# Kernel tuning notes

Measured on AMD Instinct MI355X. Metric: run time of the kernel, lower is better.

Reference implementation:

```python
import jax, jax.numpy as jnp
import numpy as np

H = 4  # pairwise_num_attention_heads

def _layer_norm(x, gamma, beta, eps=1e-5):
    mu = jnp.mean(x, axis=-1, keepdims=True)
    var = jnp.var(x, axis=-1, keepdims=True)
    return (x - mu) * jax.lax.rsqrt(var + eps) * gamma + beta

def setup_inputs() -> dict:
    key = jax.random.key(0)
    ks = jax.random.split(key, 8)
    B, L, P = 1, 256, 128
    s = 0.02
    return {
        "pairwise_states": jax.random.normal(ks[0], (B, L, L, P), jnp.float32),
        "ln_gamma": jnp.ones((P,), jnp.float32),
        "ln_beta": jnp.zeros((P,), jnp.float32),
        "Wq": jax.random.normal(ks[1], (P, P), jnp.float32) * s,
        "Wk": jax.random.normal(ks[2], (P, P), jnp.float32) * s,
        "Wv": jax.random.normal(ks[3], (P, P), jnp.float32) * s,
        "Wb": jax.random.normal(ks[4], (P, H), jnp.float32) * s,
        "Wg": jax.random.normal(ks[5], (P, P), jnp.float32) * s,
        "bg": jnp.zeros((P,), jnp.float32),
        "Wo": jax.random.normal(ks[6], (P, P), jnp.float32) * s,
        "bo": jnp.zeros((P,), jnp.float32),
    }

def reference(pairwise_states, ln_gamma, ln_beta, Wq, Wk, Wv, Wb, Wg, bg, Wo, bo):
    # Row-axis triangle attention (RibonanzaNetPairwiseAttention, axis='row', eval mode).
    B, L, _, P = pairwise_states.shape
    D = P // H  # attention_head_size
    x = _layer_norm(pairwise_states, ln_gamma, ln_beta)  # [b,i,j,p]
    q = (x @ Wq).reshape(B, L, L, H, D)
    k = (x @ Wk).reshape(B, L, L, H, D)
    v = (x @ Wv).reshape(B, L, L, H, D)
    scale = jnp.asarray(D, x.dtype) ** 0.5
    # pairwise bias: [b,i,j,h] -> broadcast over the row axis of the scores
    bias = jnp.einsum('bijp,ph->bhij', x, Wb)  # [b,h,L,L]
    # scores[b,h,i,j,k]: within row i, query position j attends to key position k
    scores = jnp.einsum('bijhd,bikhd->bhijk', q, k) / scale + bias[:, :, None]
    probs = jax.nn.softmax(scores, axis=-1)
    ctx = jnp.einsum('bhijk,bikhd->bijhd', probs, v).reshape(B, L, L, P)
    gate = jax.nn.sigmoid(x @ Wg + bg)
    ctx = gate * ctx
    # output dense + residual (AxisDropout is identity in eval mode)
    return ctx @ Wo + bo + pairwise_states
```

## Files before the change

kernel.cpp:

```cpp
#include <hip/hip_runtime.h>

#define NPOS 65536

typedef __attribute__((ext_vector_type(8))) short bf16x8;
typedef __attribute__((ext_vector_type(4))) float f32x4;

#if __has_builtin(__builtin_amdgcn_exp2f)
#define EXP2F(x) __builtin_amdgcn_exp2f(x)
#else
#define EXP2F(x) __expf((x) * 0.6931471805599453f)
#endif
#if __has_builtin(__builtin_amdgcn_rcpf)
#define RCPF(x) __builtin_amdgcn_rcpf(x)
#else
#define RCPF(x) (1.0f / (x))
#endif

static __device__ __forceinline__ unsigned short f2bf(float f) {
  union { float f; unsigned int u; } v; v.f = f;
  unsigned int r = v.u + 0x7fffu + ((v.u >> 16) & 1u);
  return (unsigned short)(r >> 16);
}
static __device__ __forceinline__ float lo_bf(unsigned int u) {
  union { unsigned int u; float f; } v; v.u = u << 16; return v.f;
}
static __device__ __forceinline__ float hi_bf(unsigned int u) {
  union { unsigned int u; float f; } v; v.u = u & 0xffff0000u; return v.f;
}
static __device__ __forceinline__ unsigned int permpack(float hi, float lo) {
  union { float f; unsigned int u; } a, b;
  a.f = hi; b.f = lo;
#if __has_builtin(__builtin_amdgcn_perm)
  return __builtin_amdgcn_perm(a.u, b.u, 0x07060302u);
#else
  return (a.u & 0xffff0000u) | (b.u >> 16);
#endif
}

__global__ void k_pack(const float* __restrict__ Wq, const float* __restrict__ Wk,
                       const float* __restrict__ Wv, const float* __restrict__ Wg,
                       const float* __restrict__ Wo,
                       ushort* __restrict__ WT, ushort* __restrict__ WoT) {
  int idx = blockIdx.x * blockDim.x + threadIdx.x;
  if (idx < 512 * 128) {
    int n = idx >> 7, k = idx & 127;
    int nn = n & 127;
    float val;
    if (n < 128)      val = Wq[k * 128 + nn] * (0.17677669529663687f * 1.4426950408889634f);
    else if (n < 256) val = Wk[k * 128 + nn];
    else if (n < 384) val = Wv[k * 128 + nn];
    else              val = Wg[k * 128 + nn];
    WT[idx] = f2bf(val);
  } else if (idx < 512 * 128 + 128 * 128) {
    int j = idx - 512 * 128;
    int n = j >> 7, k = j & 127;
    WoT[j] = f2bf(Wo[k * 128 + n]);
  }
}

__global__ __launch_bounds__(128, 4) void k_ln(
    const float* __restrict__ in, const float* __restrict__ gamma,
    const float* __restrict__ beta, const float* __restrict__ Wb,
    ushort* __restrict__ xln, ushort* __restrict__ biasB) {
  int t = threadIdx.x, wv = t >> 6, lane = t & 63;
  int n = lane & 15, g = lane >> 4;
  int myrow = blockIdx.x * 32 + wv * 16 + n;
  const float* rp = in + (size_t)myrow * 128;

  float xv[32];
  float sm = 0.f, ssm = 0.f;
  #pragma unroll
  for (int kc = 0; kc < 4; kc++)
    #pragma unroll
    for (int pr = 0; pr < 2; pr++) {
      float4 v = *(const float4*)(rp + kc * 32 + g * 8 + pr * 4);
      int o = kc * 8 + pr * 4;
      xv[o] = v.x; xv[o+1] = v.y; xv[o+2] = v.z; xv[o+3] = v.w;
      sm  += v.x + v.y + v.z + v.w;
      ssm += v.x*v.x + v.y*v.y + v.z*v.z + v.w*v.w;
    }
  sm  += __shfl_xor(sm, 16, 64);  sm  += __shfl_xor(sm, 32, 64);
  ssm += __shfl_xor(ssm, 16, 64); ssm += __shfl_xor(ssm, 32, 64);
  float mu  = sm * (1.0f / 128.0f);
  float var = ssm * (1.0f / 128.0f) - mu * mu;
  float rs  = rsqrtf(var + 1e-5f);
  float p0 = 0.f, p1 = 0.f, p2 = 0.f, p3 = 0.f;
  #pragma unroll
  for (int kc = 0; kc < 4; kc++)
    #pragma unroll
    for (int pr = 0; pr < 2; pr++) {
      int c0 = kc * 32 + g * 8 + pr * 4;
      float4 g4 = *(const float4*)(gamma + c0);
      float4 b4 = *(const float4*)(beta + c0);
      int o = kc * 8 + pr * 4;
      #pragma unroll
      for (int r = 0; r < 4; r++) {
        float xn = (xv[o + r] - mu) * rs * (&g4.x)[r] + (&b4.x)[r];
        xv[o + r] = xn;
        float4 w = ((const float4*)Wb)[c0 + r];
        p0 += xn * w.x; p1 += xn * w.y; p2 += xn * w.z; p3 += xn * w.w;
      }
    }
  #pragma unroll
  for (int kc = 0; kc < 4; kc++)
    #pragma unroll
    for (int pr = 0; pr < 2; pr++) {
      int o = kc * 8 + pr * 4;
      uint2 px;
      px.x = (unsigned int)f2bf(xv[o]) | ((unsigned int)f2bf(xv[o + 1]) << 16);
      px.y = (unsigned int)f2bf(xv[o + 2]) | ((unsigned int)f2bf(xv[o + 3]) << 16);
      *(uint2*)(xln + (size_t)myrow * 128 + kc * 32 + g * 8 + pr * 4) = px;
    }
  p0 += __shfl_xor(p0, 16, 64); p0 += __shfl_xor(p0, 32, 64);
  p1 += __shfl_xor(p1, 16, 64); p1 += __shfl_xor(p1, 32, 64);
  p2 += __shfl_xor(p2, 16, 64); p2 += __shfl_xor(p2, 32, 64);
  p3 += __shfl_xor(p3, 16, 64); p3 += __shfl_xor(p3, 32, 64);
  if (g == 0) {
    const float l2e = 1.4426950408889634f;
    biasB[0 * NPOS + myrow] = f2bf(p0 * l2e);
    biasB[1 * NPOS + myrow] = f2bf(p1 * l2e);
    biasB[2 * NPOS + myrow] = f2bf(p2 * l2e);
    biasB[3 * NPOS + myrow] = f2bf(p3 * l2e);
  }
}

#define KS 40
#define VS 264
#define PST 40
__global__ __launch_bounds__(512, 2) void k_attn2(
    const ushort* __restrict__ xln, const ushort* __restrict__ WT,
    const float* __restrict__ bg, const ushort* __restrict__ biasB,
    ushort* __restrict__ gctx) {
  __shared__ __align__(16) ushort Klds[256 * KS];
  __shared__ __align__(16) ushort VTlds[32 * VS];
  __shared__ __align__(16) ushort pstg[8][16 * PST];
  int i = blockIdx.x & 255, h = blockIdx.x >> 8;
  int t = threadIdx.x, wv = t >> 6, lane = t & 63;
  int n = lane & 15, g = lane >> 4;
  int r0 = wv * 32;

  bf16x8 a[2][4];
  const ushort* xb = xln + ((size_t)i * 256 + r0) * 128;
  #pragma unroll
  for (int c = 0; c < 2; c++)
    #pragma unroll
    for (int kc = 0; kc < 4; kc++)
      a[c][kc] = *(const bf16x8*)(xb + (size_t)(c * 16 + n) * 128 + kc * 32 + g * 8);

  bf16x8 qreg[2];
  f32x4 gs[2][2];
  #pragma unroll
  for (int sect = 0; sect < 4; sect++) {
    bf16x8 b[2][4];
    #pragma unroll
    for (int ntl = 0; ntl < 2; ntl++)
      #pragma unroll
      for (int kc = 0; kc < 4; kc++)
        b[ntl][kc] = *(const bf16x8*)(WT + (size_t)(sect * 128 + h * 32 + ntl * 16 + n) * 128 + kc * 32 + g * 8);
    #pragma unroll
    for (int c = 0; c < 2; c++) {
      f32x4 acc[2];
      #pragma unroll
      for (int ntl = 0; ntl < 2; ntl++) {
        f32x4 cc = {0.f, 0.f, 0.f, 0.f};
        #pragma unroll
        for (int kc = 0; kc < 4; kc++) {
          if (sect == 0)
            cc = __builtin_amdgcn_mfma_f32_16x16x32_bf16(b[ntl][kc], a[c][kc], cc, 0, 0, 0);
          else
            cc = __builtin_amdgcn_mfma_f32_16x16x32_bf16(a[c][kc], b[ntl][kc], cc, 0, 0, 0);
        }
        acc[ntl] = cc;
      }
      if (sect == 0) {
        union { bf16x8 v; uint2 u[2]; } q;
        q.u[0].x = permpack(acc[0][1], acc[0][0]);
        q.u[0].y = permpack(acc[0][3], acc[0][2]);
        q.u[1].x = permpack(acc[1][1], acc[1][0]);
        q.u[1].y = permpack(acc[1][3], acc[1][2]);
        qreg[c] = q.v;
      } else if (sect == 1) {
        #pragma unroll
        for (int ntl = 0; ntl < 2; ntl++)
          #pragma unroll
          for (int r = 0; r < 4; r++)
            Klds[(r0 + c * 16 + g * 4 + r) * KS + ntl * 16 + n] = f2bf(acc[ntl][r]);
      } else if (sect == 2) {
        #pragma unroll
        for (int ntl = 0; ntl < 2; ntl++) {
          uint2 vp;
          vp.x = (unsigned int)f2bf(acc[ntl][0]) | ((unsigned int)f2bf(acc[ntl][1]) << 16);
          vp.y = (unsigned int)f2bf(acc[ntl][2]) | ((unsigned int)f2bf(acc[ntl][3]) << 16);
          *(uint2*)(&VTlds[(ntl * 16 + n) * VS + r0 + c * 16 + g * 4]) = vp;
        }
      } else {
        #pragma unroll
        for (int ntl = 0; ntl < 2; ntl++)
          #pragma unroll
          for (int r = 0; r < 4; r++)
            gs[c][ntl][r] = 1.0f / (1.0f + __expf(-(acc[ntl][r] + bg[h * 32 + ntl * 16 + n])));
      }
    }
  }
  __syncthreads();

  const ushort* bb = biasB + (size_t)h * NPOS;
  ushort* Pw = pstg[wv];
  #pragma unroll
  for (int tt = 0; tt < 2; tt++) {
    int j0 = r0 + tt * 16;
    uint2 bv[16];
    #pragma unroll
    for (int kt = 0; kt < 16; kt++)
      bv[kt] = *(const uint2*)(bb + (size_t)(j0 + n) * 256 + kt * 16 + g * 4);
    f32x4 s[16];
    #pragma unroll
    for (int kt = 0; kt < 16; kt++) {
      union { bf16x8 v; uint2 u[2]; } ak;
      ak.u[0] = *(const uint2*)(&Klds[(kt * 16 + n) * KS + g * 4]);
      ak.u[1] = *(const uint2*)(&Klds[(kt * 16 + n) * KS + 16 + g * 4]);
      f32x4 cc;
      cc[0] = lo_bf(bv[kt].x); cc[1] = hi_bf(bv[kt].x);
      cc[2] = lo_bf(bv[kt].y); cc[3] = hi_bf(bv[kt].y);
      s[kt] = __builtin_amdgcn_mfma_f32_16x16x32_bf16(ak.v, qreg[tt], cc, 0, 0, 0);
    }
    f32x4 a4 = {0.f, 0.f, 0.f, 0.f};
    #pragma unroll
    for (int kt = 0; kt < 16; kt++) {
      #pragma unroll
      for (int r = 0; r < 4; r++) s[kt][r] = EXP2F(s[kt][r]);
      a4 += s[kt];
    }
    float smm = (a4[0] + a4[1]) + (a4[2] + a4[3]);
    smm += __shfl_xor(smm, 16, 64);
    smm += __shfl_xor(smm, 32, 64);
    float inv = RCPF(smm);
    f32x4 ctx0 = {0.f, 0.f, 0.f, 0.f}, ctx1 = {0.f, 0.f, 0.f, 0.f};
    #pragma unroll
    for (int c8 = 0; c8 < 8; c8++) {
      #pragma unroll
      for (int t2 = 0; t2 < 2; t2++) {
        int kt = c8 * 2 + t2;
        uint2 pp;
        pp.x = permpack(s[kt][1] * inv, s[kt][0] * inv);
        pp.y = permpack(s[kt][3] * inv, s[kt][2] * inv);
        *(uint2*)(&Pw[n * PST + t2 * 16 + g * 4]) = pp;
      }
      bf16x8 ap = *(const bf16x8*)(&Pw[n * PST + g * 8]);
      bf16x8 v0 = *(const bf16x8*)(&VTlds[(size_t)n * VS + c8 * 32 + g * 8]);
      bf16x8 v1 = *(const bf16x8*)(&VTlds[(size_t)(16 + n) * VS + c8 * 32 + g * 8]);
      ctx0 = __builtin_amdgcn_mfma_f32_16x16x32_bf16(ap, v0, ctx0, 0, 0, 0);
      ctx1 = __builtin_amdgcn_mfma_f32_16x16x32_bf16(ap, v1, ctx1, 0, 0, 0);
    }
    #pragma unroll
    for (int r = 0; r < 4; r++) {
      size_t pos = (size_t)i * 256 + j0 + g * 4 + r;
      gctx[pos * 128 + h * 32 + n]      = f2bf(ctx0[r] * gs[tt][0][r]);
      gctx[pos * 128 + h * 32 + 16 + n] = f2bf(ctx1[r] * gs[tt][1][r]);
    }
  }
}

__global__ __launch_bounds__(256, 4) void k_out(
    const ushort* __restrict__ gctx, const ushort* __restrict__ WoT,
    const float* __restrict__ bo, const float* __restrict__ in0,
    float* __restrict__ out) {
  int t = threadIdx.x, wv = t >> 6, lane = t & 63;
  int n = lane & 15, g = lane >> 4;
  int row0 = blockIdx.x * 64 + wv * 16;
  bf16x8 cfr[4];
  #pragma unroll
  for (int kc = 0; kc < 4; kc++)
    cfr[kc] = *(const bf16x8*)(gctx + (size_t)(row0 + n) * 128 + kc * 32 + g * 8);
  size_t rowg = (size_t)row0 + n;
  #pragma unroll
  for (int ntl = 0; ntl < 8; ntl++) {
    f32x4 acc = {0.f, 0.f, 0.f, 0.f};
    #pragma unroll
    for (int kc = 0; kc < 4; kc++) {
      bf16x8 wo = *(const bf16x8*)(WoT + (size_t)(ntl * 16 + n) * 128 + kc * 32 + g * 8);
      acc = __builtin_amdgcn_mfma_f32_16x16x32_bf16(wo, cfr[kc], acc, 0, 0, 0);
    }
    f32x4 b4 = *(const f32x4*)(bo + ntl * 16 + g * 4);
    size_t o = rowg * 128 + ntl * 16 + g * 4;
    f32x4 r4 = *(const f32x4*)(in0 + o);
    acc[0] += b4[0] + r4[0]; acc[1] += b4[1] + r4[1];
    acc[2] += b4[2] + r4[2]; acc[3] += b4[3] + r4[3];
    *(f32x4*)(out + o) = acc;
  }
}

extern "C" void kernel_launch(void* const* d_in, const int* in_sizes, int n_in,
                              void* d_out, int out_size, void* d_ws, size_t ws_size,
                              hipStream_t stream) {
  const float* in0   = (const float*)d_in[0];
  const float* gamma = (const float*)d_in[1];
  const float* beta  = (const float*)d_in[2];
  const float* Wq    = (const float*)d_in[3];
  const float* Wk    = (const float*)d_in[4];
  const float* Wv    = (const float*)d_in[5];
  const float* Wb    = (const float*)d_in[6];
  const float* Wg    = (const float*)d_in[7];
  const float* bg    = (const float*)d_in[8];
  const float* Wo    = (const float*)d_in[9];
  const float* bo    = (const float*)d_in[10];
  float* out = (float*)d_out;
  char* ws = (char*)d_ws;

  const size_t MB = 1024 * 1024;
  ushort* gctx  = (ushort*)(ws);
  ushort* xln   = (ushort*)(ws + 16 * MB);
  ushort* biasB = (ushort*)(ws + 32 * MB);
  ushort* WT    = (ushort*)(ws + 33 * MB);
  ushort* WoT   = (ushort*)(ws + 33 * MB + 128 * 1024);

  k_pack <<<320, 256, 0, stream>>>(Wq, Wk, Wv, Wg, Wo, WT, WoT);
  k_ln   <<<2048, 128, 0, stream>>>(in0, gamma, beta, Wb, xln, biasB);
  k_attn2<<<1024, 512, 0, stream>>>(xln, WT, bg, biasB, gctx);
  k_out  <<<1024, 256, 0, stream>>>(gctx, WoT, bo, in0, out);
}
```

Before: 219.6 us.

## Merge weight packing into LN kernel and stage Q through LDS

Folds the weight-packing kernel into the layer-norm kernel as extra blocks, which removes one kernel launch and lets the packing run concurrently with normalization. The LN output is now written with 16-byte stores instead of 8-byte ones. In the attention kernel, Q is no longer built as a transposed-MFMA register fragment. It is written to a per-wave LDS staging buffer and read back as one bf16x8, and K is read with a single 16-byte LDS load. The cost is extra shared memory per block and an extra LDS round trip for Q, which could lower occupancy.

Measured after the change: 201.2 us. 1.09x faster.

```diff
diff --git a/kernel.cpp b/kernel.cpp
--- a/kernel.cpp
+++ b/kernel.cpp
@@ -37,32 +37,34 @@
 #endif
 }
 
-__global__ void k_pack(const float* __restrict__ Wq, const float* __restrict__ Wk,
-                       const float* __restrict__ Wv, const float* __restrict__ Wg,
-                       const float* __restrict__ Wo,
-                       ushort* __restrict__ WT, ushort* __restrict__ WoT) {
-  int idx = blockIdx.x * blockDim.x + threadIdx.x;
-  if (idx < 512 * 128) {
-    int n = idx >> 7, k = idx & 127;
-    int nn = n & 127;
-    float val;
-    if (n < 128)      val = Wq[k * 128 + nn] * (0.17677669529663687f * 1.4426950408889634f);
-    else if (n < 256) val = Wk[k * 128 + nn];
-    else if (n < 384) val = Wv[k * 128 + nn];
-    else              val = Wg[k * 128 + nn];
-    WT[idx] = f2bf(val);
-  } else if (idx < 512 * 128 + 128 * 128) {
-    int j = idx - 512 * 128;
-    int n = j >> 7, k = j & 127;
-    WoT[j] = f2bf(Wo[k * 128 + n]);
-  }
-}
-
-__global__ __launch_bounds__(128, 4) void k_ln(
+__global__ __launch_bounds__(128, 4) void k_lnpack(
     const float* __restrict__ in, const float* __restrict__ gamma,
     const float* __restrict__ beta, const float* __restrict__ Wb,
-    ushort* __restrict__ xln, ushort* __restrict__ biasB) {
-  int t = threadIdx.x, wv = t >> 6, lane = t & 63;
+    const float* __restrict__ Wq, const float* __restrict__ Wk,
+    const float* __restrict__ Wv, const float* __restrict__ Wg,
+    const float* __restrict__ Wo,
+    ushort* __restrict__ xln, ushort* __restrict__ biasB,
+    ushort* __restrict__ WT, ushort* __restrict__ WoT) {
+  int t = threadIdx.x;
+  if (blockIdx.x >= 2048) {
+    int idx = (blockIdx.x - 2048) * 128 + t;
+    if (idx < 512 * 128) {
+      int n = idx >> 7, k = idx & 127;
+      int nn = n & 127;
+      float val;
+      if (n < 128)      val = Wq[k * 128 + nn] * (0.17677669529663687f * 1.4426950408889634f);
+      else if (n < 256) val = Wk[k * 128 + nn];
+      else if (n < 384) val = Wv[k * 128 + nn];
+      else              val = Wg[k * 128 + nn];
+      WT[idx] = f2bf(val);
+    } else {
+      int j = idx - 512 * 128;
+      int n = j >> 7, k = j & 127;
+      WoT[j] = f2bf(Wo[k * 128 + n]);
+    }
+    return;
+  }
+  int wv = t >> 6, lane = t & 63;
   int n = lane & 15, g = lane >> 4;
   int myrow = blockIdx.x * 32 + wv * 16 + n;
   const float* rp = in + (size_t)myrow * 128;
@@ -102,15 +104,15 @@
       }
     }
   #pragma unroll
-  for (int kc = 0; kc < 4; kc++)
-    #pragma unroll
-    for (int pr = 0; pr < 2; pr++) {
-      int o = kc * 8 + pr * 4;
-      uint2 px;
-      px.x = (unsigned int)f2bf(xv[o]) | ((unsigned int)f2bf(xv[o + 1]) << 16);
-      px.y = (unsigned int)f2bf(xv[o + 2]) | ((unsigned int)f2bf(xv[o + 3]) << 16);
-      *(uint2*)(xln + (size_t)myrow * 128 + kc * 32 + g * 8 + pr * 4) = px;
-    }
+  for (int kc = 0; kc < 4; kc++) {
+    int o = kc * 8;
+    uint4 px;
+    px.x = (unsigned int)f2bf(xv[o])     | ((unsigned int)f2bf(xv[o + 1]) << 16);
+    px.y = (unsigned int)f2bf(xv[o + 2]) | ((unsigned int)f2bf(xv[o + 3]) << 16);
+    px.z = (unsigned int)f2bf(xv[o + 4]) | ((unsigned int)f2bf(xv[o + 5]) << 16);
+    px.w = (unsigned int)f2bf(xv[o + 6]) | ((unsigned int)f2bf(xv[o + 7]) << 16);
+    *(uint4*)(xln + (size_t)myrow * 128 + kc * 32 + g * 8) = px;
+  }
   p0 += __shfl_xor(p0, 16, 64); p0 += __shfl_xor(p0, 32, 64);
   p1 += __shfl_xor(p1, 16, 64); p1 += __shfl_xor(p1, 32, 64);
   p2 += __shfl_xor(p2, 16, 64); p2 += __shfl_xor(p2, 32, 64);
@@ -126,6 +128,7 @@
 
 #define KS 40
 #define VS 264
+#define QS 40
 #define PST 40
 __global__ __launch_bounds__(512, 2) void k_attn2(
     const ushort* __restrict__ xln, const ushort* __restrict__ WT,
@@ -133,6 +136,7 @@
     ushort* __restrict__ gctx) {
   __shared__ __align__(16) ushort Klds[256 * KS];
   __shared__ __align__(16) ushort VTlds[32 * VS];
+  __shared__ __align__(16) ushort qstg[8][32 * QS];
   __shared__ __align__(16) ushort pstg[8][16 * PST];
   int i = blockIdx.x & 255, h = blockIdx.x >> 8;
   int t = threadIdx.x, wv = t >> 6, lane = t & 63;
@@ -147,7 +151,6 @@
     for (int kc = 0; kc < 4; kc++)
       a[c][kc] = *(const bf16x8*)(xb + (size_t)(c * 16 + n) * 128 + kc * 32 + g * 8);
 
-  bf16x8 qreg[2];
   f32x4 gs[2][2];
   #pragma unroll
   for (int sect = 0; sect < 4; sect++) {
@@ -164,21 +167,16 @@
       for (int ntl = 0; ntl < 2; ntl++) {
         f32x4 cc = {0.f, 0.f, 0.f, 0.f};
         #pragma unroll
-        for (int kc = 0; kc < 4; kc++) {
-          if (sect == 0)
-            cc = __builtin_amdgcn_mfma_f32_16x16x32_bf16(b[ntl][kc], a[c][kc], cc, 0, 0, 0);
-          else
-            cc = __builtin_amdgcn_mfma_f32_16x16x32_bf16(a[c][kc], b[ntl][kc], cc, 0, 0, 0);
-        }
+        for (int kc = 0; kc < 4; kc++)
+          cc = __builtin_amdgcn_mfma_f32_16x16x32_bf16(a[c][kc], b[ntl][kc], cc, 0, 0, 0);
         acc[ntl] = cc;
       }
       if (sect == 0) {
-        union { bf16x8 v; uint2 u[2]; } q;
-        q.u[0].x = permpack(acc[0][1], acc[0][0]);
-        q.u[0].y = permpack(acc[0][3], acc[0][2]);
-        q.u[1].x = permpack(acc[1][1], acc[1][0]);
-        q.u[1].y = permpack(acc[1][3], acc[1][2]);
-        qreg[c] = q.v;
+        #pragma unroll
+        for (int ntl = 0; ntl < 2; ntl++)
+          #pragma unroll
+          for (int r = 0; r < 4; r++)
+            qstg[wv][(c * 16 + g * 4 + r) * QS + ntl * 16 + n] = f2bf(acc[ntl][r]);
       } else if (sect == 1) {
         #pragma unroll
         for (int ntl = 0; ntl < 2; ntl++)
@@ -209,6 +207,7 @@
   #pragma unroll
   for (int tt = 0; tt < 2; tt++) {
     int j0 = r0 + tt * 16;
+    bf16x8 bq = *(const bf16x8*)(&qstg[wv][(tt * 16 + n) * QS + g * 8]);
     uint2 bv[16];
     #pragma unroll
     for (int kt = 0; kt < 16; kt++)
@@ -216,13 +215,11 @@
     f32x4 s[16];
     #pragma unroll
     for (int kt = 0; kt < 16; kt++) {
-      union { bf16x8 v; uint2 u[2]; } ak;
-      ak.u[0] = *(const uint2*)(&Klds[(kt * 16 + n) * KS + g * 4]);
-      ak.u[1] = *(const uint2*)(&Klds[(kt * 16 + n) * KS + 16 + g * 4]);
+      bf16x8 ak = *(const bf16x8*)(&Klds[(kt * 16 + n) * KS + g * 8]);
       f32x4 cc;
       cc[0] = lo_bf(bv[kt].x); cc[1] = hi_bf(bv[kt].x);
       cc[2] = lo_bf(bv[kt].y); cc[3] = hi_bf(bv[kt].y);
-      s[kt] = __builtin_amdgcn_mfma_f32_16x16x32_bf16(ak.v, qreg[tt], cc, 0, 0, 0);
+      s[kt] = __builtin_amdgcn_mfma_f32_16x16x32_bf16(ak, bq, cc, 0, 0, 0);
     }
     f32x4 a4 = {0.f, 0.f, 0.f, 0.f};
     #pragma unroll
@@ -314,8 +311,8 @@
   ushort* WT    = (ushort*)(ws + 33 * MB);
   ushort* WoT   = (ushort*)(ws + 33 * MB + 128 * 1024);
 
-  k_pack <<<320, 256, 0, stream>>>(Wq, Wk, Wv, Wg, Wo, WT, WoT);
-  k_ln   <<<2048, 128, 0, stream>>>(in0, gamma, beta, Wb, xln, biasB);
-  k_attn2<<<1024, 512, 0, stream>>>(xln, WT, bg, biasB, gctx);
-  k_out  <<<1024, 256, 0, stream>>>(gctx, WoT, bo, in0, out);
-}
+  k_lnpack<<<2688, 128, 0, stream>>>(in0, gamma, beta, Wb, Wq, Wk, Wv, Wg, Wo,
+                                     xln, biasB, WT, WoT);
+  k_attn2 <<<1024, 512, 0, stream>>>(xln, WT, bg, biasB, gctx);
+  k_out   <<<1024, 256, 0, stream>>>(gctx, WoT, bo, in0, out);
+}
```
